# Kernel optimization log

Hardware: AMD Instinct MI355X
Metric: run time of the kernel (lower is better)

Reference implementation:

```python
import jax, jax.numpy as jnp
import numpy as np

B, H, W, D = 64, 56, 56, 128
WS = 7            # window size per axis
NH = 4            # attention heads
L = 2             # transformer layers (layer 1 is shifted)
HID = 4 * D
G1, G2 = H // WS, W // WS
G, N = G1 * G2, WS * WS
SH = WS // 2      # cyclic shift


def _build_attn_mask():
    # faithful port of ShiftWindow mask construction (numpy constants)
    img = np.zeros((H, W), dtype=np.float32)
    sl = (slice(0, -WS), slice(-WS, -SH), slice(-SH, None))
    idx = 0
    for s0 in sl:
        for s1 in sl:
            img[s0, s1] = idx
            idx += 1
    win = img.reshape(G1, WS, G2, WS).transpose(0, 2, 1, 3).reshape(G, N)
    diff = win[:, None, :] - win[:, :, None]          # [G, N, N]
    return jnp.asarray(np.where(diff != 0, -100.0, 0.0).astype(np.float32))

ATTN_MASK = _build_attn_mask()


def setup_inputs() -> dict:
    key = jax.random.key(0)
    ks = jax.random.split(key, 8)
    s = 0.02
    return {
        'x': jax.random.normal(ks[0], (B, H, W, D), jnp.float32),
        'ln1_g': jnp.ones((L, D)), 'ln1_b': jnp.zeros((L, D)),
        'qkv_w': s * jax.random.normal(ks[1], (L, D, 3 * D)), 'qkv_b': jnp.zeros((L, 3 * D)),
        'proj_w': s * jax.random.normal(ks[2], (L, D, D)), 'proj_b': jnp.zeros((L, D)),
        'ln2_g': jnp.ones((L, D)), 'ln2_b': jnp.zeros((L, D)),
        'mlp_w1': s * jax.random.normal(ks[3], (L, D, HID)), 'mlp_b1': jnp.zeros((L, HID)),
        'mlp_w2': s * jax.random.normal(ks[4], (L, HID, D)), 'mlp_b2': jnp.zeros((L, D)),
        'ds_norm_g': jnp.ones((4 * D,)), 'ds_norm_b': jnp.zeros((4 * D,)),
        'ds_w': s * jax.random.normal(ks[5], (4 * D, 2 * D)),
    }


def _ln(x, g, b, eps=1e-5):
    m = jnp.mean(x, -1, keepdims=True)
    v = jnp.mean((x - m) ** 2, -1, keepdims=True)
    return (x - m) * jax.lax.rsqrt(v + eps) * g + b


def _partition(x):
    # [B, H, W, D] -> [B, G, N, D]
    x = x.reshape(B, G1, WS, G2, WS, D).transpose(0, 1, 3, 2, 4, 5)
    return x.reshape(B, G, N, D)


def _unpartition(xw):
    x = xw.reshape(B, G1, G2, WS, WS, D).transpose(0, 1, 3, 2, 4, 5)
    return x.reshape(B, H, W, D)


def _block(xw, mask, i, p):
    # pre-norm window attention
    h = _ln(xw, p['ln1_g'][i], p['ln1_b'][i])
    qkv = h @ p['qkv_w'][i] + p['qkv_b'][i]                 # [B,G,N,3D]
    q, k, v = jnp.split(qkv, 3, axis=-1)
    hd = D // NH
    q = q.reshape(B, G, N, NH, hd)
    k = k.reshape(B, G, N, NH, hd)
    v = v.reshape(B, G, N, NH, hd)
    scores = jnp.einsum('bgnhd,bgmhd->bghnm', q, k) / jnp.sqrt(jnp.float32(hd))
    if mask is not None:
        scores = scores + mask[None, :, None, :, :]         # [1,G,1,N,N]
    attn = jax.nn.softmax(scores, axis=-1)
    o = jnp.einsum('bghnm,bgmhd->bgnhd', attn, v).reshape(B, G, N, D)
    xw = xw + o @ p['proj_w'][i] + p['proj_b'][i]
    # MLP
    h = _ln(xw, p['ln2_g'][i], p['ln2_b'][i])
    h = jax.nn.gelu(h @ p['mlp_w1'][i] + p['mlp_b1'][i])
    return xw + h @ p['mlp_w2'][i] + p['mlp_b2'][i]


def reference(x, ln1_g, ln1_b, qkv_w, qkv_b, proj_w, proj_b, ln2_g, ln2_b,
              mlp_w1, mlp_b1, mlp_w2, mlp_b2, ds_norm_g, ds_norm_b, ds_w):
    p = dict(ln1_g=ln1_g, ln1_b=ln1_b, qkv_w=qkv_w, qkv_b=qkv_b,
             proj_w=proj_w, proj_b=proj_b, ln2_g=ln2_g, ln2_b=ln2_b,
             mlp_w1=mlp_w1, mlp_b1=mlp_b1, mlp_w2=mlp_w2, mlp_b2=mlp_b2)
    xw = _partition(x)
    for i in range(L):
        shift = (i % 2 == 1)
        if shift:
            xw = _partition(jnp.roll(_unpartition(xw), (-SH, -SH), axis=(1, 2)))
            xw = _block(xw, ATTN_MASK, i, p)
            xw = _partition(jnp.roll(_unpartition(xw), (SH, SH), axis=(1, 2)))
        else:
            xw = _block(xw, None, i, p)
    x = _unpartition(xw)
    # Downsample: 2x2 patch merge -> LN -> Linear(4D -> 2D) (no bias)
    x = x.reshape(B, H // 2, 2, W // 2, 2, D).transpose(0, 1, 3, 2, 4, 5)
    x = x.reshape(B, H // 2, W // 2, 4 * D)
    x = _ln(x, ds_norm_g, ds_norm_b) @ ds_w
    return x
```

## Files before the change

kernel.cpp:

```cpp
#include <hip/hip_runtime.h>
#include <hip/hip_bf16.h>


typedef short bf16x8 __attribute__((ext_vector_type(8)));
typedef float f32x4 __attribute__((ext_vector_type(4)));
typedef unsigned short u16;
typedef unsigned int u32;

#define MTOK 200704
#define DSTOK 50176

__device__ __forceinline__ u16 f2b(float f){
  u32 u = __float_as_uint(f);
  u += 0x7fffu + ((u >> 16) & 1u);
  return (u16)(u >> 16);
}
__device__ __forceinline__ float blo(u32 u){ return __uint_as_float(u << 16); }
__device__ __forceinline__ float bhi(u32 u){ return __uint_as_float(u & 0xffff0000u); }
__device__ __forceinline__ float b2f(u16 u){ return __uint_as_float(((u32)u) << 16); }

__device__ __forceinline__ float gelu_tanh(float v){
  float u = 0.7978845608028654f * (v + 0.044715f * v * v * v);
  u = fminf(u, 10.f);
  float e = __expf(2.f * u);
  float t = (e - 1.f) / (e + 1.f);
  return 0.5f * v * (1.f + t);
}

#define GLDS(gp, lp) __builtin_amdgcn_global_load_lds( \
    (const __attribute__((address_space(1))) u32*)(gp), \
    (__attribute__((address_space(3))) u32*)(lp), 16, 0, 0)

__global__ void transpose_cvt(const float* __restrict__ src, u16* __restrict__ dst,
                              int K, int N){
  int e = blockIdx.x * 256 + threadIdx.x;
  if (e >= K * N) return;
  int k = e / N, n = e - k * N;
  dst[n * K + k] = f2b(src[e]);
}

__global__ __launch_bounds__(256) void ln0_kernel(const float* __restrict__ src,
    const float* __restrict__ gw, const float* __restrict__ bw,
    u16* __restrict__ dst)
{
  int wv = threadIdx.x >> 6, lane = threadIdx.x & 63;
  int t = blockIdx.x * 4 + wv;
  int n = t % 49; int tq = t / 49; int gg = tq & 63; int b_ = tq >> 6;
  int r = n / 7, c = n - 7 * r;
  int h = (gg >> 3) * 7 + r, w = (gg & 7) * 7 + c;
  long soff = ((long)((b_ * 56 + h) * 56 + w)) * 128;
  float2 v = *(const float2*)(src + soff + lane * 2);
  float s = v.x + v.y, s2 = v.x * v.x + v.y * v.y;
  #pragma unroll
  for (int o = 32; o; o >>= 1) { s += __shfl_xor(s, o); s2 += __shfl_xor(s2, o); }
  float mean = s * 0.0078125f;
  float var  = s2 * 0.0078125f - mean * mean;
  float rstd = rsqrtf(var + 1e-5f);
  int c0 = lane * 2;
  ushort2 o2;
  o2.x = f2b((v.x - mean) * rstd * gw[c0]   + bw[c0]);
  o2.y = f2b((v.y - mean) * rstd * gw[c0+1] + bw[c0+1]);
  *(ushort2*)(dst + (long)t * 128 + c0) = o2;
}

__global__ __launch_bounds__(256) void ds_ln_kernel(const u16* __restrict__ x,
    const float* __restrict__ gw, const float* __restrict__ bw,
    u16* __restrict__ dst)
{
  int wv = threadIdx.x >> 6, lane = threadIdx.x & 63;
  int t = blockIdx.x * 4 + wv;
  int j = t % 28; int tq = t / 28; int i = tq % 28; int b_ = tq / 28;
  int e0 = lane * 8;
  int p = e0 >> 8, q = (e0 >> 7) & 1, d = e0 & 127;
  const u16* src = x + ((long)((b_ * 56 + 2*i + p) * 56 + 2*j + q)) * 128 + d;
  uint4 a = *(const uint4*)src;
  float vs[8] = {blo(a.x), bhi(a.x), blo(a.y), bhi(a.y),
                 blo(a.z), bhi(a.z), blo(a.w), bhi(a.w)};
  float s = 0.f, s2 = 0.f;
  #pragma unroll
  for (int u = 0; u < 8; u++) { s += vs[u]; s2 += vs[u] * vs[u]; }
  #pragma unroll
  for (int o = 32; o; o >>= 1) { s += __shfl_xor(s, o); s2 += __shfl_xor(s2, o); }
  float mean = s * (1.f / 512.f);
  float var  = s2 * (1.f / 512.f) - mean * mean;
  float rstd = rsqrtf(var + 1e-5f);
  u16 ov[8];
  #pragma unroll
  for (int u = 0; u < 8; u++) ov[u] = f2b((vs[u] - mean) * rstd * gw[e0+u] + bw[e0+u]);
  uint4 o4;
  o4.x = (u32)ov[0] | ((u32)ov[1] << 16);
  o4.y = (u32)ov[2] | ((u32)ov[3] << 16);
  o4.z = (u32)ov[4] | ((u32)ov[5] << 16);
  o4.w = (u32)ov[6] | ((u32)ov[7] << 16);
  *(uint4*)(dst + (long)t * 512 + e0) = o4;
}

template<int MASKED>
__global__ __launch_bounds__(256) void attn_mfma(const u16* __restrict__ qkv,
                                                 u16* __restrict__ obuf)
{
  __shared__ u16 Pls_all[4][64][72];
  const int h = threadIdx.x >> 6;
  const int lane = threadIdx.x & 63;
  const int c = lane & 15, g = lane >> 4;
  const int wi = blockIdx.x;
  const int g_ = wi & 63;
  const long t0 = (long)wi * 49;
  u16 (*Pls)[72] = Pls_all[h];

  bf16x8 qf[4], kf[4];
  #pragma unroll
  for (int mi = 0; mi < 4; mi++) {
    int r = 16*mi + c; r = r > 48 ? 48 : r;
    qf[mi] = *(const bf16x8*)(qkv + (t0 + r)*384 + h*32 + g*8);
  }
  #pragma unroll
  for (int ni = 0; ni < 4; ni++) {
    int r = 16*ni + c; r = r > 48 ? 48 : r;
    kf[ni] = *(const bf16x8*)(qkv + (t0 + r)*384 + 128 + h*32 + g*8);
  }

  f32x4 acc[4][4];
  const f32x4 zero4 = {0.f, 0.f, 0.f, 0.f};
  #pragma unroll
  for (int mi = 0; mi < 4; mi++)
    #pragma unroll
    for (int ni = 0; ni < 4; ni++)
      acc[mi][ni] = __builtin_amdgcn_mfma_f32_16x16x32_bf16(qf[mi], kf[ni], zero4, 0, 0, 0);

  bf16x8 vf[2][2];
  #pragma unroll
  for (int ni2 = 0; ni2 < 2; ni2++)
    #pragma unroll
    for (int ks = 0; ks < 2; ks++)
      #pragma unroll
      for (int jj = 0; jj < 8; jj++) {
        int k = ks*32 + 8*g + jj; k = k > 48 ? 48 : k;
        vf[ni2][ks][jj] = (short)qkv[(t0 + k)*384 + 256 + h*32 + 16*ni2 + c];
      }

  int rid_c[4];
  int g1b = 0, g2b = 0;
  if (MASKED) {
    g1b = (g_ >> 3) * 7; g2b = (g_ & 7) * 7;
    #pragma unroll
    for (int ni = 0; ni < 4; ni++) {
      int col = 16*ni + c; col = col > 48 ? 48 : col;
      int cr = col / 7, cc = col - 7*cr;
      int hh = g1b + cr, ww = g2b + cc;
      rid_c[ni] = (hh < 49 ? 0 : (hh < 53 ? 1 : 2)) * 3 + (ww < 49 ? 0 : (ww < 53 ? 1 : 2));
    }
  }

  #pragma unroll
  for (int mi = 0; mi < 4; mi++) {
    #pragma unroll
    for (int j = 0; j < 4; j++) {
      int rr = 16*mi + 4*g + j;
      int rid_r = 0;
      if (MASKED) {
        int r2 = rr > 48 ? 48 : rr;
        int rh = r2 / 7, rw = r2 - 7*rh;
        int hh = g1b + rh, ww = g2b + rw;
        rid_r = (hh < 49 ? 0 : (hh < 53 ? 1 : 2)) * 3 + (ww < 49 ? 0 : (ww < 53 ? 1 : 2));
      }
      float sv[4];
      #pragma unroll
      for (int ni = 0; ni < 4; ni++) {
        float s = acc[mi][ni][j] * 0.17677669529663687f;
        int col = 16*ni + c;
        if (col >= 49) s = -1e30f;
        else if (MASKED && rid_c[ni] != rid_r) s -= 100.f;
        sv[ni] = s;
      }
      float m4 = fmaxf(fmaxf(sv[0], sv[1]), fmaxf(sv[2], sv[3]));
      #pragma unroll
      for (int o = 1; o <= 8; o <<= 1) m4 = fmaxf(m4, __shfl_xor(m4, o));
      float p[4], sum = 0.f;
      #pragma unroll
      for (int ni = 0; ni < 4; ni++) { p[ni] = __expf(sv[ni] - m4); sum += p[ni]; }
      #pragma unroll
      for (int o = 1; o <= 8; o <<= 1) sum += __shfl_xor(sum, o);
      float rs = 1.f / sum;
      #pragma unroll
      for (int ni = 0; ni < 4; ni++)
        Pls[rr][16*ni + c] = f2b(p[ni] * rs);
    }
  }

  __syncthreads();

  f32x4 accO[4][2];
  #pragma unroll
  for (int mi = 0; mi < 4; mi++)
    #pragma unroll
    for (int ni2 = 0; ni2 < 2; ni2++) accO[mi][ni2] = zero4;
  #pragma unroll
  for (int mi = 0; mi < 4; mi++)
    #pragma unroll
    for (int ks = 0; ks < 2; ks++) {
      bf16x8 pa = *(const bf16x8*)(&Pls[16*mi + c][ks*32 + g*8]);
      #pragma unroll
      for (int ni2 = 0; ni2 < 2; ni2++)
        accO[mi][ni2] = __builtin_amdgcn_mfma_f32_16x16x32_bf16(pa, vf[ni2][ks], accO[mi][ni2], 0, 0, 0);
    }

  #pragma unroll
  for (int mi = 0; mi < 4; mi++)
    #pragma unroll
    for (int ni2 = 0; ni2 < 2; ni2++)
      #pragma unroll
      for (int j = 0; j < 4; j++) {
        int r = 16*mi + 4*g + j;
        if (r < 49)
          obuf[(t0 + r)*128 + h*32 + 16*ni2 + c] = f2b(accO[mi][ni2][j]);
      }
}

template<int K, int EPI, int RESF32>
__global__ __launch_bounds__(256) void gemm_kernel(
    const u16* __restrict__ A, const u16* __restrict__ Bt,
    const float* __restrict__ bias, int Ntot,
    u16* __restrict__ outb, float* __restrict__ outf,
    u16* __restrict__ outx, const float* __restrict__ resf, int shift,
    const float* __restrict__ lng, const float* __restrict__ lnb,
    u16* __restrict__ lnout)
{
  __shared__ __align__(16) u16 sh[16384];
  u16* Asl = sh;
  u16* Bsl = sh + 8192;
  float (*Cf)[128] = (float(*)[128])sh;

  const int tid = threadIdx.x;
  const int row0 = blockIdx.x * 128, col0 = blockIdx.y * 128;
  const int wv = tid >> 6, lane = tid & 63;
  const int m_off = (wv >> 1) * 64, n_off = (wv & 1) * 64;
  const int lr = lane & 15, lk = (lane >> 4) * 8;

  f32x4 acc[4][4];
  const f32x4 zero4 = {0.f, 0.f, 0.f, 0.f};
  #pragma unroll
  for (int a1 = 0; a1 < 4; a1++)
    #pragma unroll
    for (int a2 = 0; a2 < 4; a2++) acc[a1][a2] = zero4;

  for (int k0 = 0; k0 < K; k0 += 64) {
    __syncthreads();
    #pragma unroll
    for (int j = 0; j < 4; j++) {
      int ch = tid + j * 256;
      int r = ch >> 3, cc = ch & 7;
      int col = k0 + ((cc * 8) ^ ((r & 7) << 3));
      GLDS(A  + (long)(row0 + r) * K + col, Asl + ch * 8);
      GLDS(Bt + (long)(col0 + r) * K + col, Bsl + ch * 8);
    }
    __syncthreads();
    #pragma unroll
    for (int kk = 0; kk < 64; kk += 32) {
      bf16x8 af[4], bfr[4];
      #pragma unroll
      for (int mi = 0; mi < 4; mi++) {
        int R = m_off + mi*16 + lr;
        af[mi] = *(const bf16x8*)&Asl[R*64 + ((kk + lk) ^ ((R & 7) << 3))];
      }
      #pragma unroll
      for (int ni = 0; ni < 4; ni++) {
        int R = n_off + ni*16 + lr;
        bfr[ni] = *(const bf16x8*)&Bsl[R*64 + ((kk + lk) ^ ((R & 7) << 3))];
      }
      #pragma unroll
      for (int mi = 0; mi < 4; mi++)
        #pragma unroll
        for (int ni = 0; ni < 4; ni++)
          acc[mi][ni] = __builtin_amdgcn_mfma_f32_16x16x32_bf16(
              af[mi], bfr[ni], acc[mi][ni], 0, 0, 0);
    }
  }

  const int g = lane >> 4;
  #pragma unroll
  for (int half = 0; half < 2; half++) {
    __syncthreads();
    if ((wv >> 1) == half) {
      #pragma unroll
      for (int mi = 0; mi < 4; mi++)
        #pragma unroll
        for (int ni = 0; ni < 4; ni++)
          #pragma unroll
          for (int j = 0; j < 4; j++) {
            int lrow = mi*16 + 4*g + j;
            int col  = n_off + ni*16 + lr;
            Cf[lrow][col ^ ((lrow & 7) << 2)] = acc[mi][ni][j];
          }
    }
    __syncthreads();
    #pragma unroll
    for (int jj = 0; jj < 8; jj++) {
      int ch = tid + jj * 256;
      int r = ch >> 5, c4 = ch & 31;
      float4 v = *(const float4*)&Cf[r][(c4*4) ^ ((r & 7) << 2)];
      int grow = row0 + half*64 + r;
      int gcol = col0 + c4*4;
      if (EPI == 0) {
        float4 b4 = *(const float4*)&bias[gcol];
        uint2 o2;
        o2.x = (u32)f2b(v.x + b4.x) | ((u32)f2b(v.y + b4.y) << 16);
        o2.y = (u32)f2b(v.z + b4.z) | ((u32)f2b(v.w + b4.w) << 16);
        *(uint2*)(outb + (long)grow * Ntot + gcol) = o2;
      } else if (EPI == 2) {
        int n = grow % 49; int tq = grow / 49; int gg = tq & 63; int b_ = tq >> 6;
        int rr = n / 7, cc = n - 7 * rr;
        int hh = (gg >> 3) * 7 + rr, ww = (gg & 7) * 7 + cc;
        if (shift) { hh += 3; if (hh >= 56) hh -= 56; ww += 3; if (ww >= 56) ww -= 56; }
        long t = (long)(b_ * 56 + hh) * 56 + ww;
        long obase = t * 128;
        float4 b4 = *(const float4*)&bias[gcol];
        float r0, r1, r2, r3;
        if (RESF32) {
          float4 res = *(const float4*)&resf[obase + gcol];
          r0 = res.x; r1 = res.y; r2 = res.z; r3 = res.w;
        } else {
          uint2 cur = *(const uint2*)&outx[obase + gcol];
          r0 = blo(cur.x); r1 = bhi(cur.x); r2 = blo(cur.y); r3 = bhi(cur.y);
        }
        float o0 = r0 + v.x + b4.x, o1 = r1 + v.y + b4.y;
        float o2v = r2 + v.z + b4.z, o3 = r3 + v.w + b4.w;
        uint2 xw;
        xw.x = (u32)f2b(o0) | ((u32)f2b(o1) << 16);
        xw.y = (u32)f2b(o2v) | ((u32)f2b(o3) << 16);
        *(uint2*)(outx + obase + gcol) = xw;
        float s = o0 + o1 + o2v + o3;
        float s2 = o0*o0 + o1*o1 + o2v*o2v + o3*o3;
        #pragma unroll
        for (int o = 1; o <= 16; o <<= 1) { s += __shfl_xor(s, o); s2 += __shfl_xor(s2, o); }
        float mean = s * 0.0078125f;
        float var  = s2 * 0.0078125f - mean * mean;
        float rstd = rsqrtf(var + 1e-5f);
        float4 g4 = *(const float4*)&lng[gcol];
        float4 bb4 = *(const float4*)&lnb[gcol];
        uint2 lo2;
        lo2.x = (u32)f2b((o0 - mean) * rstd * g4.x + bb4.x) |
                ((u32)f2b((o1 - mean) * rstd * g4.y + bb4.y) << 16);
        lo2.y = (u32)f2b((o2v - mean) * rstd * g4.z + bb4.z) |
                ((u32)f2b((o3 - mean) * rstd * g4.w + bb4.w) << 16);
        *(uint2*)(lnout + obase + gcol) = lo2;
      } else {
        *(float4*)&outf[(long)grow * Ntot + gcol] = v;
      }
    }
  }
}

template<int WRITE_LN>
__global__ __launch_bounds__(256) void mlp_kernel(
    const u16* __restrict__ xh, const u16* __restrict__ w1t, const float* __restrict__ b1,
    const u16* __restrict__ w2t, const float* __restrict__ b2,
    u16* __restrict__ xrmw,
    const float* __restrict__ lng, const float* __restrict__ lnb,
    u16* __restrict__ lnout)
{
  __shared__ __align__(16) u16 S0[16384];
  __shared__ __align__(16) u16 S1[16384];
  const int tid = threadIdx.x;
  const int row0 = blockIdx.x * 128;
  const int wv = tid >> 6, lane = tid & 63;
  const int m_off = (wv >> 1) * 64, n_off = (wv & 1) * 64;
  const int lr = lane & 15, lk = (lane >> 4) * 8, g = lane >> 4;

  f32x4 acc_o[4][4];
  const f32x4 zero4 = {0.f, 0.f, 0.f, 0.f};
  #pragma unroll
  for (int a1 = 0; a1 < 4; a1++)
    #pragma unroll
    for (int a2 = 0; a2 < 4; a2++) acc_o[a1][a2] = zero4;

  for (int nc = 0; nc < 4; nc++) {
    __syncthreads();
    #pragma unroll
    for (int j = 0; j < 8; j++) {
      int ch = tid + j * 256;
      int r = ch >> 4, cc = ch & 15;
      int col = (cc * 8) ^ ((r & 7) << 3);
      GLDS(xh  + (long)(row0 + r) * 128 + col,      S0 + ch * 8);
      GLDS(w1t + (long)(nc * 128 + r) * 128 + col,  S1 + ch * 8);
    }
    __syncthreads();
    f32x4 acc_h[4][4];
    #pragma unroll
    for (int a1 = 0; a1 < 4; a1++)
      #pragma unroll
      for (int a2 = 0; a2 < 4; a2++) acc_h[a1][a2] = zero4;
    #pragma unroll
    for (int kk = 0; kk < 128; kk += 32) {
      bf16x8 af[4], bfr[4];
      #pragma unroll
      for (int mi = 0; mi < 4; mi++) {
        int R = m_off + mi*16 + lr;
        af[mi] = *(const bf16x8*)&S0[R*128 + ((kk + lk) ^ ((R & 7) << 3))];
      }
      #pragma unroll
      for (int ni = 0; ni < 4; ni++) {
        int R = n_off + ni*16 + lr;
        bfr[ni] = *(const bf16x8*)&S1[R*128 + ((kk + lk) ^ ((R & 7) << 3))];
      }
      #pragma unroll
      for (int mi = 0; mi < 4; mi++)
        #pragma unroll
        for (int ni = 0; ni < 4; ni++)
          acc_h[mi][ni] = __builtin_amdgcn_mfma_f32_16x16x32_bf16(
              af[mi], bfr[ni], acc_h[mi][ni], 0, 0, 0);
    }
    __syncthreads();
    #pragma unroll
    for (int mi = 0; mi < 4; mi++)
      #pragma unroll
      for (int ni = 0; ni < 4; ni++)
        #pragma unroll
        for (int j = 0; j < 4; j++) {
          int lrow = m_off + mi*16 + 4*g + j;
          int col  = n_off + ni*16 + lr;
          float hv = gelu_tanh(acc_h[mi][ni][j] + b1[nc*128 + col]);
          S0[lrow*128 + (col ^ ((lrow & 7) << 3))] = f2b(hv);
        }
    #pragma unroll
    for (int j = 0; j < 8; j++) {
      int ch = tid + j * 256;
      int r = ch >> 4, cc = ch & 15;
      int col = (cc * 8) ^ ((r & 7) << 3);
      GLDS(w2t + (long)r * 512 + nc * 128 + col, S1 + ch * 8);
    }
    __syncthreads();
    #pragma unroll
    for (int kk = 0; kk < 128; kk += 32) {
      bf16x8 af[4], bfr[4];
      #pragma unroll
      for (int mi = 0; mi < 4; mi++) {
        int R = m_off + mi*16 + lr;
        af[mi] = *(const bf16x8*)&S0[R*128 + ((kk + lk) ^ ((R & 7) << 3))];
      }
      #pragma unroll
      for (int ni = 0; ni < 4; ni++) {
        int R = n_off + ni*16 + lr;
        bfr[ni] = *(const bf16x8*)&S1[R*128 + ((kk + lk) ^ ((R & 7) << 3))];
      }
      #pragma unroll
      for (int mi = 0; mi < 4; mi++)
        #pragma unroll
        for (int ni = 0; ni < 4; ni++)
          acc_o[mi][ni] = __builtin_amdgcn_mfma_f32_16x16x32_bf16(
              af[mi], bfr[ni], acc_o[mi][ni], 0, 0, 0);
    }
  }

  float (*Cf)[128] = (float(*)[128])S0;
  #pragma unroll
  for (int half = 0; half < 2; half++) {
    __syncthreads();
    if ((wv >> 1) == half) {
      #pragma unroll
      for (int mi = 0; mi < 4; mi++)
        #pragma unroll
        for (int ni = 0; ni < 4; ni++)
          #pragma unroll
          for (int j = 0; j < 4; j++) {
            int lrow = mi*16 + 4*g + j;
            int col  = n_off + ni*16 + lr;
            Cf[lrow][col ^ ((lrow & 7) << 2)] = acc_o[mi][ni][j];
          }
    }
    __syncthreads();
    #pragma unroll
    for (int jj = 0; jj < 8; jj++) {
      int ch = tid + jj * 256;
      int r = ch >> 5, c4 = ch & 31;
      float4 v = *(const float4*)&Cf[r][(c4*4) ^ ((r & 7) << 2)];
      int t = row0 + half*64 + r;
      int gcol = c4*4;
      float4 b4 = *(const float4*)&b2[gcol];
      uint2 cur = *(const uint2*)&xrmw[(long)t * 128 + gcol];
      float o0 = blo(cur.x) + v.x + b4.x;
      float o1 = bhi(cur.x) + v.y + b4.y;
      float o2v = blo(cur.y) + v.z + b4.z;
      float o3 = bhi(cur.y) + v.w + b4.w;
      uint2 xw;
      xw.x = (u32)f2b(o0) | ((u32)f2b(o1) << 16);
      xw.y = (u32)f2b(o2v) | ((u32)f2b(o3) << 16);
      *(uint2*)(xrmw + (long)t * 128 + gcol) = xw;
      if (WRITE_LN) {
        float s = o0 + o1 + o2v + o3;
        float s2 = o0*o0 + o1*o1 + o2v*o2v + o3*o3;
        #pragma unroll
        for (int o = 1; o <= 16; o <<= 1) { s += __shfl_xor(s, o); s2 += __shfl_xor(s2, o); }
        float mean = s * 0.0078125f;
        float var  = s2 * 0.0078125f - mean * mean;
        float rstd = rsqrtf(var + 1e-5f);
        float4 g4  = *(const float4*)&lng[gcol];
        float4 bb4 = *(const float4*)&lnb[gcol];
        int b_ = t / 3136; int rem = t - b_ * 3136;
        int hh = rem / 56, ww = rem - hh * 56;
        int hs = hh + 53; if (hs >= 56) hs -= 56;
        int ws = ww + 53; if (ws >= 56) ws -= 56;
        int gg = (hs / 7) * 8 + (ws / 7);
        int nn = (hs % 7) * 7 + (ws % 7);
        long dst = ((long)(b_ * 64 + gg) * 49 + nn) * 128 + gcol;
        uint2 lo2;
        lo2.x = (u32)f2b((o0 - mean) * rstd * g4.x + bb4.x) |
                ((u32)f2b((o1 - mean) * rstd * g4.y + bb4.y) << 16);
        lo2.y = (u32)f2b((o2v - mean) * rstd * g4.z + bb4.z) |
                ((u32)f2b((o3 - mean) * rstd * g4.w + bb4.w) << 16);
        *(uint2*)(lnout + dst) = lo2;
      }
    }
  }
}

extern "C" void kernel_launch(void* const* d_in, const int* in_sizes, int n_in,
                              void* d_out, int out_size, void* d_ws, size_t ws_size,
                              hipStream_t stream)
{
  const float* x_in   = (const float*)d_in[0];
  const float* ln1_g  = (const float*)d_in[1];
  const float* ln1_b  = (const float*)d_in[2];
  const float* qkv_w  = (const float*)d_in[3];
  const float* qkv_b  = (const float*)d_in[4];
  const float* proj_w = (const float*)d_in[5];
  const float* proj_b = (const float*)d_in[6];
  const float* ln2_g  = (const float*)d_in[7];
  const float* ln2_b  = (const float*)d_in[8];
  const float* w1     = (const float*)d_in[9];
  const float* b1     = (const float*)d_in[10];
  const float* w2     = (const float*)d_in[11];
  const float* b2     = (const float*)d_in[12];
  const float* dsg    = (const float*)d_in[13];
  const float* dsb    = (const float*)d_in[14];
  const float* dsw    = (const float*)d_in[15];

  u16* x_ws     = (u16*)d_ws;
  u16* buf_h    = x_ws + (long)MTOK * 128;
  u16* xh       = buf_h + (long)MTOK * 128;
  u16* buf_big  = xh + (long)MTOK * 128;
  u16* wts      = buf_big + (long)MTOK * 512;
  u16* qkv_wt   = wts;
  u16* proj_wt  = qkv_wt  + 2 * 49152;
  u16* w1t      = proj_wt + 2 * 16384;
  u16* w2t      = w1t     + 2 * 65536;
  u16* ds_wt    = w2t     + 2 * 65536;

  for (int i = 0; i < 2; i++) {
    transpose_cvt<<<(49152+255)/256, 256, 0, stream>>>(qkv_w  + i*49152, qkv_wt  + i*49152, 128, 384);
    transpose_cvt<<<(16384+255)/256, 256, 0, stream>>>(proj_w + i*16384, proj_wt + i*16384, 128, 128);
    transpose_cvt<<<(65536+255)/256, 256, 0, stream>>>(w1     + i*65536, w1t     + i*65536, 128, 512);
    transpose_cvt<<<(65536+255)/256, 256, 0, stream>>>(w2     + i*65536, w2t     + i*65536, 512, 128);
  }
  transpose_cvt<<<(131072+255)/256, 256, 0, stream>>>(dsw, ds_wt, 512, 256);

  ln0_kernel<<<MTOK/4, 256, 0, stream>>>(x_in, ln1_g, ln1_b, buf_h);
  gemm_kernel<128,0,0><<<dim3(MTOK/128, 3), 256, 0, stream>>>(
      buf_h, qkv_wt, qkv_b, 384, buf_big, nullptr, nullptr, nullptr, 0,
      nullptr, nullptr, nullptr);
  attn_mfma<0><<<4096, 256, 0, stream>>>(buf_big, buf_h);
  gemm_kernel<128,2,1><<<dim3(MTOK/128, 1), 256, 0, stream>>>(
      buf_h, proj_wt, proj_b, 128, nullptr, nullptr, x_ws, x_in, 0,
      ln2_g, ln2_b, xh);
  mlp_kernel<1><<<MTOK/128, 256, 0, stream>>>(
      xh, w1t, b1, w2t, b2, x_ws, ln1_g + 128, ln1_b + 128, buf_h);

  gemm_kernel<128,0,0><<<dim3(MTOK/128, 3), 256, 0, stream>>>(
      buf_h, qkv_wt + 49152, qkv_b + 384, 384, buf_big, nullptr, nullptr, nullptr, 0,
      nullptr, nullptr, nullptr);
  attn_mfma<1><<<4096, 256, 0, stream>>>(buf_big, buf_h);
  gemm_kernel<128,2,0><<<dim3(MTOK/128, 1), 256, 0, stream>>>(
      buf_h, proj_wt + 16384, proj_b + 128, 128, nullptr, nullptr, x_ws, nullptr, 1,
      ln2_g + 128, ln2_b + 128, xh);
  mlp_kernel<0><<<MTOK/128, 256, 0, stream>>>(
      xh, w1t + 65536, b1 + 512, w2t + 65536, b2 + 128, x_ws,
      nullptr, nullptr, nullptr);

  ds_ln_kernel<<<DSTOK/4, 256, 0, stream>>>(x_ws, dsg, dsb, buf_big);
  gemm_kernel<512,4,0><<<dim3(DSTOK/128, 2), 256, 0, stream>>>(
      buf_big, ds_wt, nullptr, 256, nullptr, (float*)d_out, nullptr, nullptr, 0,
      nullptr, nullptr, nullptr);
}
```

Measured before the change: 1.227 ms.

## Restructure MLP kernel to per-wave token tiles with register-resident activations

```diff
diff --git a/kernel.cpp b/kernel.cpp
--- a/kernel.cpp
+++ b/kernel.cpp
@@ -17,7 +17,6 @@
 }
 __device__ __forceinline__ float blo(u32 u){ return __uint_as_float(u << 16); }
 __device__ __forceinline__ float bhi(u32 u){ return __uint_as_float(u & 0xffff0000u); }
-__device__ __forceinline__ float b2f(u16 u){ return __uint_as_float(((u32)u) << 16); }
 
 __device__ __forceinline__ float gelu_tanh(float v){
   float u = 0.7978845608028654f * (v + 0.044715f * v * v * v);
@@ -359,156 +358,118 @@
     const float* __restrict__ lng, const float* __restrict__ lnb,
     u16* __restrict__ lnout)
 {
-  __shared__ __align__(16) u16 S0[16384];
-  __shared__ __align__(16) u16 S1[16384];
+  __shared__ __align__(16) u16 Hls_all[4][4096];
   const int tid = threadIdx.x;
-  const int row0 = blockIdx.x * 128;
   const int wv = tid >> 6, lane = tid & 63;
-  const int m_off = (wv >> 1) * 64, n_off = (wv & 1) * 64;
-  const int lr = lane & 15, lk = (lane >> 4) * 8, g = lane >> 4;
-
-  f32x4 acc_o[4][4];
+  const int lr = lane & 15, g = lane >> 4;
+  const int row0 = blockIdx.x * 128 + wv * 32;
+  char* Hb = (char*)Hls_all[wv];
+
+  bf16x8 tf[2][4];
+  #pragma unroll
+  for (int nit = 0; nit < 2; nit++)
+    #pragma unroll
+    for (int ks = 0; ks < 4; ks++)
+      tf[nit][ks] = *(const bf16x8*)(xh + (long)(row0 + nit*16 + lr) * 128 + ks*32 + g*8);
+
+  f32x4 acc_o[8][2];
   const f32x4 zero4 = {0.f, 0.f, 0.f, 0.f};
   #pragma unroll
-  for (int a1 = 0; a1 < 4; a1++)
-    #pragma unroll
-    for (int a2 = 0; a2 < 4; a2++) acc_o[a1][a2] = zero4;
+  for (int mo = 0; mo < 8; mo++) { acc_o[mo][0] = zero4; acc_o[mo][1] = zero4; }
+
+  const int tok0 = lr, tok1 = 16 + lr;
+  const int sw0 = (tok0 & 7) << 4, sw1 = (tok1 & 7) << 4;
 
   for (int nc = 0; nc < 4; nc++) {
-    __syncthreads();
-    #pragma unroll
-    for (int j = 0; j < 8; j++) {
-      int ch = tid + j * 256;
-      int r = ch >> 4, cc = ch & 15;
-      int col = (cc * 8) ^ ((r & 7) << 3);
-      GLDS(xh  + (long)(row0 + r) * 128 + col,      S0 + ch * 8);
-      GLDS(w1t + (long)(nc * 128 + r) * 128 + col,  S1 + ch * 8);
-    }
-    __syncthreads();
-    f32x4 acc_h[4][4];
-    #pragma unroll
-    for (int a1 = 0; a1 < 4; a1++)
-      #pragma unroll
-      for (int a2 = 0; a2 < 4; a2++) acc_h[a1][a2] = zero4;
-    #pragma unroll
-    for (int kk = 0; kk < 128; kk += 32) {
-      bf16x8 af[4], bfr[4];
-      #pragma unroll
-      for (int mi = 0; mi < 4; mi++) {
-        int R = m_off + mi*16 + lr;
-        af[mi] = *(const bf16x8*)&S0[R*128 + ((kk + lk) ^ ((R & 7) << 3))];
-      }
-      #pragma unroll
-      for (int ni = 0; ni < 4; ni++) {
-        int R = n_off + ni*16 + lr;
-        bfr[ni] = *(const bf16x8*)&S1[R*128 + ((kk + lk) ^ ((R & 7) << 3))];
-      }
-      #pragma unroll
-      for (int mi = 0; mi < 4; mi++)
-        #pragma unroll
-        for (int ni = 0; ni < 4; ni++)
-          acc_h[mi][ni] = __builtin_amdgcn_mfma_f32_16x16x32_bf16(
-              af[mi], bfr[ni], acc_h[mi][ni], 0, 0, 0);
-    }
-    __syncthreads();
-    #pragma unroll
-    for (int mi = 0; mi < 4; mi++)
-      #pragma unroll
-      for (int ni = 0; ni < 4; ni++)
-        #pragma unroll
-        for (int j = 0; j < 4; j++) {
-          int lrow = m_off + mi*16 + 4*g + j;
-          int col  = n_off + ni*16 + lr;
-          float hv = gelu_tanh(acc_h[mi][ni][j] + b1[nc*128 + col]);
-          S0[lrow*128 + (col ^ ((lrow & 7) << 3))] = f2b(hv);
-        }
-    #pragma unroll
-    for (int j = 0; j < 8; j++) {
-      int ch = tid + j * 256;
-      int r = ch >> 4, cc = ch & 15;
-      int col = (cc * 8) ^ ((r & 7) << 3);
-      GLDS(w2t + (long)r * 512 + nc * 128 + col, S1 + ch * 8);
-    }
-    __syncthreads();
-    #pragma unroll
-    for (int kk = 0; kk < 128; kk += 32) {
-      bf16x8 af[4], bfr[4];
-      #pragma unroll
-      for (int mi = 0; mi < 4; mi++) {
-        int R = m_off + mi*16 + lr;
-        af[mi] = *(const bf16x8*)&S0[R*128 + ((kk + lk) ^ ((R & 7) << 3))];
-      }
-      #pragma unroll
-      for (int ni = 0; ni < 4; ni++) {
-        int R = n_off + ni*16 + lr;
-        bfr[ni] = *(const bf16x8*)&S1[R*128 + ((kk + lk) ^ ((R & 7) << 3))];
-      }
-      #pragma unroll
-      for (int mi = 0; mi < 4; mi++)
-        #pragma unroll
-        for (int ni = 0; ni < 4; ni++)
-          acc_o[mi][ni] = __builtin_amdgcn_mfma_f32_16x16x32_bf16(
-              af[mi], bfr[ni], acc_o[mi][ni], 0, 0, 0);
-    }
-  }
-
-  float (*Cf)[128] = (float(*)[128])S0;
-  #pragma unroll
-  for (int half = 0; half < 2; half++) {
-    __syncthreads();
-    if ((wv >> 1) == half) {
-      #pragma unroll
-      for (int mi = 0; mi < 4; mi++)
-        #pragma unroll
-        for (int ni = 0; ni < 4; ni++)
-          #pragma unroll
-          for (int j = 0; j < 4; j++) {
-            int lrow = mi*16 + 4*g + j;
-            int col  = n_off + ni*16 + lr;
-            Cf[lrow][col ^ ((lrow & 7) << 2)] = acc_o[mi][ni][j];
-          }
-    }
-    __syncthreads();
-    #pragma unroll
-    for (int jj = 0; jj < 8; jj++) {
-      int ch = tid + jj * 256;
-      int r = ch >> 5, c4 = ch & 31;
-      float4 v = *(const float4*)&Cf[r][(c4*4) ^ ((r & 7) << 2)];
-      int t = row0 + half*64 + r;
-      int gcol = c4*4;
-      float4 b4 = *(const float4*)&b2[gcol];
-      uint2 cur = *(const uint2*)&xrmw[(long)t * 128 + gcol];
-      float o0 = blo(cur.x) + v.x + b4.x;
-      float o1 = bhi(cur.x) + v.y + b4.y;
-      float o2v = blo(cur.y) + v.z + b4.z;
-      float o3 = bhi(cur.y) + v.w + b4.w;
+    #pragma unroll
+    for (int mh = 0; mh < 8; mh++) {
+      bf16x8 wf[4];
+      #pragma unroll
+      for (int ks = 0; ks < 4; ks++)
+        wf[ks] = *(const bf16x8*)(w1t + (long)(nc*128 + mh*16 + lr) * 128 + ks*32 + g*8);
+      f32x4 ah0 = zero4, ah1 = zero4;
+      #pragma unroll
+      for (int ks = 0; ks < 4; ks++) {
+        ah0 = __builtin_amdgcn_mfma_f32_16x16x32_bf16(wf[ks], tf[0][ks], ah0, 0, 0, 0);
+        ah1 = __builtin_amdgcn_mfma_f32_16x16x32_bf16(wf[ks], tf[1][ks], ah1, 0, 0, 0);
+      }
+      float4 b4 = *(const float4*)(b1 + nc*128 + mh*16 + 4*g);
+      int colb = mh*32 + 8*g;
+      uint2 hp;
+      hp.x = (u32)f2b(gelu_tanh(ah0[0] + b4.x)) | ((u32)f2b(gelu_tanh(ah0[1] + b4.y)) << 16);
+      hp.y = (u32)f2b(gelu_tanh(ah0[2] + b4.z)) | ((u32)f2b(gelu_tanh(ah0[3] + b4.w)) << 16);
+      *(uint2*)(Hb + tok0*256 + (colb ^ sw0)) = hp;
+      hp.x = (u32)f2b(gelu_tanh(ah1[0] + b4.x)) | ((u32)f2b(gelu_tanh(ah1[1] + b4.y)) << 16);
+      hp.y = (u32)f2b(gelu_tanh(ah1[2] + b4.z)) | ((u32)f2b(gelu_tanh(ah1[3] + b4.w)) << 16);
+      *(uint2*)(Hb + tok1*256 + (colb ^ sw1)) = hp;
+    }
+    bf16x8 hb0[4], hb1[4];
+    #pragma unroll
+    for (int ks = 0; ks < 4; ks++) {
+      int cb = ks*64 + g*16;
+      hb0[ks] = *(const bf16x8*)(Hb + tok0*256 + (cb ^ sw0));
+      hb1[ks] = *(const bf16x8*)(Hb + tok1*256 + (cb ^ sw1));
+    }
+    #pragma unroll
+    for (int mo = 0; mo < 8; mo++) {
+      bf16x8 wf[4];
+      #pragma unroll
+      for (int ks = 0; ks < 4; ks++)
+        wf[ks] = *(const bf16x8*)(w2t + (long)(mo*16 + lr) * 512 + nc*128 + ks*32 + g*8);
+      #pragma unroll
+      for (int ks = 0; ks < 4; ks++) {
+        acc_o[mo][0] = __builtin_amdgcn_mfma_f32_16x16x32_bf16(wf[ks], hb0[ks], acc_o[mo][0], 0, 0, 0);
+        acc_o[mo][1] = __builtin_amdgcn_mfma_f32_16x16x32_bf16(wf[ks], hb1[ks], acc_o[mo][1], 0, 0, 0);
+      }
+    }
+  }
+
+  #pragma unroll
+  for (int nit = 0; nit < 2; nit++) {
+    long t = row0 + nit*16 + lr;
+    float s = 0.f, s2 = 0.f;
+    float ov[8][4];
+    #pragma unroll
+    for (int mo = 0; mo < 8; mo++) {
+      float4 b4 = *(const float4*)(b2 + mo*16 + 4*g);
+      uint2 cur = *(const uint2*)(xrmw + t*128 + mo*16 + 4*g);
+      float o0  = blo(cur.x) + acc_o[mo][nit][0] + b4.x;
+      float o1  = bhi(cur.x) + acc_o[mo][nit][1] + b4.y;
+      float o2v = blo(cur.y) + acc_o[mo][nit][2] + b4.z;
+      float o3  = bhi(cur.y) + acc_o[mo][nit][3] + b4.w;
       uint2 xw;
-      xw.x = (u32)f2b(o0) | ((u32)f2b(o1) << 16);
+      xw.x = (u32)f2b(o0)  | ((u32)f2b(o1) << 16);
       xw.y = (u32)f2b(o2v) | ((u32)f2b(o3) << 16);
-      *(uint2*)(xrmw + (long)t * 128 + gcol) = xw;
+      *(uint2*)(xrmw + t*128 + mo*16 + 4*g) = xw;
       if (WRITE_LN) {
-        float s = o0 + o1 + o2v + o3;
-        float s2 = o0*o0 + o1*o1 + o2v*o2v + o3*o3;
-        #pragma unroll
-        for (int o = 1; o <= 16; o <<= 1) { s += __shfl_xor(s, o); s2 += __shfl_xor(s2, o); }
-        float mean = s * 0.0078125f;
-        float var  = s2 * 0.0078125f - mean * mean;
-        float rstd = rsqrtf(var + 1e-5f);
-        float4 g4  = *(const float4*)&lng[gcol];
-        float4 bb4 = *(const float4*)&lnb[gcol];
-        int b_ = t / 3136; int rem = t - b_ * 3136;
-        int hh = rem / 56, ww = rem - hh * 56;
-        int hs = hh + 53; if (hs >= 56) hs -= 56;
-        int ws = ww + 53; if (ws >= 56) ws -= 56;
-        int gg = (hs / 7) * 8 + (ws / 7);
-        int nn = (hs % 7) * 7 + (ws % 7);
-        long dst = ((long)(b_ * 64 + gg) * 49 + nn) * 128 + gcol;
-        uint2 lo2;
-        lo2.x = (u32)f2b((o0 - mean) * rstd * g4.x + bb4.x) |
-                ((u32)f2b((o1 - mean) * rstd * g4.y + bb4.y) << 16);
-        lo2.y = (u32)f2b((o2v - mean) * rstd * g4.z + bb4.z) |
-                ((u32)f2b((o3 - mean) * rstd * g4.w + bb4.w) << 16);
-        *(uint2*)(lnout + dst) = lo2;
+        ov[mo][0] = o0; ov[mo][1] = o1; ov[mo][2] = o2v; ov[mo][3] = o3;
+        s  += o0 + o1 + o2v + o3;
+        s2 += o0*o0 + o1*o1 + o2v*o2v + o3*o3;
+      }
+    }
+    if (WRITE_LN) {
+      s  += __shfl_xor(s, 16);  s2 += __shfl_xor(s2, 16);
+      s  += __shfl_xor(s, 32);  s2 += __shfl_xor(s2, 32);
+      float mean = s * 0.0078125f;
+      float var  = s2 * 0.0078125f - mean * mean;
+      float rstd = rsqrtf(var + 1e-5f);
+      int b_ = (int)(t / 3136); int rem = (int)t - b_ * 3136;
+      int hh = rem / 56, ww = rem - hh * 56;
+      int hs = hh + 53; if (hs >= 56) hs -= 56;
+      int ws = ww + 53; if (ws >= 56) ws -= 56;
+      int gg = (hs / 7) * 8 + (ws / 7);
+      int nn = (hs % 7) * 7 + (ws % 7);
+      long dst = ((long)(b_ * 64 + gg) * 49 + nn) * 128;
+      #pragma unroll
+      for (int mo = 0; mo < 8; mo++) {
+        float4 g4 = *(const float4*)(lng + mo*16 + 4*g);
+        float4 bb = *(const float4*)(lnb + mo*16 + 4*g);
+        uint2 lo;
+        lo.x = (u32)f2b((ov[mo][0] - mean) * rstd * g4.x + bb.x) |
+               ((u32)f2b((ov[mo][1] - mean) * rstd * g4.y + bb.y) << 16);
+        lo.y = (u32)f2b((ov[mo][2] - mean) * rstd * g4.z + bb.z) |
+               ((u32)f2b((ov[mo][3] - mean) * rstd * g4.w + bb.w) << 16);
+        *(uint2*)(lnout + dst + mo*16 + 4*g) = lo;
       }
     }
   }
```

Result: slower. 1.302 ms (+6.1%).
